# Optimization experiments

Hardware: AMD Instinct MI355X
Metric: run time of the kernel (lower is better)

The kernel has to match this reference:

```python
import jax, jax.numpy as jnp
import numpy as np

N, DIM, H, E = 50000, 64, 8, 800000
NEG_SLOPE = 0.2


def setup_inputs() -> dict:
    key = jax.random.key(0)
    ks = jax.random.split(key, 6)
    x = jax.random.normal(ks[0], (N, DIM), dtype=jnp.float32)
    edge_index = jax.random.randint(ks[1], (2, E), 0, N, dtype=jnp.int32)
    # glorot-ish scaled params
    W = jax.random.normal(ks[2], (DIM, H * DIM), dtype=jnp.float32) * (1.0 / np.sqrt(DIM))
    att_src = jax.random.normal(ks[3], (H, DIM), dtype=jnp.float32) * (1.0 / np.sqrt(DIM))
    att_dst = jax.random.normal(ks[4], (H, DIM), dtype=jnp.float32) * (1.0 / np.sqrt(DIM))
    bias = jnp.zeros((DIM,), dtype=jnp.float32)
    return {"x": x, "edge_index": edge_index, "W": W, "att_src": att_src, "att_dst": att_dst, "bias": bias}


def reference(x, edge_index, W, att_src, att_dst, bias):
    n = x.shape[0]
    # PyG GATConv default: add self-loops
    loops = jnp.arange(n, dtype=edge_index.dtype)
    src = jnp.concatenate([edge_index[0], loops])  # [E+N]
    dst = jnp.concatenate([edge_index[1], loops])  # [E+N]
    # project: [N, H, C]
    h = (x @ W).reshape(n, H, DIM)
    # per-node attention contributions: [N, H]
    a_src = jnp.einsum("nhc,hc->nh", h, att_src)
    a_dst = jnp.einsum("nhc,hc->nh", h, att_dst)
    # per-edge logits with LeakyReLU: [E+N, H]
    logits = jax.nn.leaky_relu(a_src[src] + a_dst[dst], negative_slope=NEG_SLOPE)
    # segment softmax over incoming edges of each destination node
    seg_max = jax.ops.segment_max(logits, dst, num_segments=n)  # [N, H]
    seg_max = jnp.where(jnp.isfinite(seg_max), seg_max, 0.0)
    e = jnp.exp(logits - seg_max[dst])
    denom = jax.ops.segment_sum(e, dst, num_segments=n)  # [N, H]
    alpha = e / denom[dst]  # every node has a self-loop -> denom > 0
    # weighted messages and scatter-add: [E+N, H, C] -> [N, H, C]
    msg = h[src] * alpha[:, :, None]
    out = jax.ops.segment_sum(msg, dst, num_segments=n)
    # concat=False -> mean over heads, then bias
    return out.mean(axis=1) + bias
```

## Files before the change

kernel.cpp:

```cpp
#include <hip/hip_runtime.h>
#include <hip/hip_bf16.h>

#define NHEAD 8
#define KDIM 64
#define NCOL 512
#define NEG_SLOPE 0.2f
#define BUCKET 62
#define ROWS 64
#define EPT 16

typedef short bf16x8 __attribute__((ext_vector_type(8)));
typedef float f32x4 __attribute__((ext_vector_type(4)));

__device__ inline float leaky(float x) { return fmaxf(x, NEG_SLOPE * x); }
__device__ inline float bf2f(unsigned short u) { return __uint_as_float(((unsigned)u) << 16); }
__device__ inline unsigned short f2bf(float f) {
    unsigned b = __float_as_uint(f);
    b += 0x7FFFu + ((b >> 16) & 1u);
    return (unsigned short)(b >> 16);
}

__global__ void k_wprep(const float* __restrict__ W, const float* __restrict__ att_src,
                        const float* __restrict__ att_dst,
                        float* __restrict__ WsT, float* __restrict__ WdT,
                        unsigned short* __restrict__ Bhi, unsigned short* __restrict__ Blo,
                        unsigned short* __restrict__ bucket, int n) {
    int tid = blockIdx.x * 256 + threadIdx.x;
    for (int i = tid; i < n; i += 32768) *(int*)(bucket + (size_t)i * ROWS) = 0;
    if (tid < NHEAD * KDIM) {
        int h = tid >> 6, k = tid & 63;
        float ps = 0.f, pd = 0.f;
        const float4* wp = (const float4*)(W + (size_t)k * NCOL + h * KDIM);
        const float4* sp = (const float4*)(att_src + h * KDIM);
        const float4* dp = (const float4*)(att_dst + h * KDIM);
        #pragma unroll
        for (int q = 0; q < KDIM / 4; ++q) {
            float4 wv = wp[q], sv = sp[q], dv = dp[q];
            ps += wv.x * sv.x + wv.y * sv.y + wv.z * sv.z + wv.w * sv.w;
            pd += wv.x * dv.x + wv.y * dv.y + wv.z * dv.z + wv.w * dv.w;
        }
        WsT[h * KDIM + k] = ps;
        WdT[h * KDIM + k] = pd;
    }
    if (tid < 4 * 16 * 64 * 8) {
        int j  = tid & 7;
        int l  = (tid >> 3) & 63;
        int kk = (tid >> 9) & 15;
        int ct = tid >> 13;
        int c  = ct * 16 + (l & 15);
        int hk = kk * 32 + ((l >> 4) << 3) + j;
        int h = hk >> 6, kx = hk & 63;
        float w = W[(size_t)kx * NCOL + h * KDIM + c];
        unsigned short hi = f2bf(w);
        Bhi[tid] = hi;
        Blo[tid] = f2bf(w - bf2f(hi));
    }
}

__global__ void k_xafill(const float* __restrict__ x,
                         const int* __restrict__ src, const int* __restrict__ dst,
                         const float* __restrict__ WsT, const float* __restrict__ WdT,
                         float* __restrict__ asrc, float* __restrict__ adst,
                         unsigned short* __restrict__ xb,
                         unsigned short* __restrict__ bucket,
                         int n, int E, int nbx) {
    const int b = blockIdx.x;
    const int t = threadIdx.x;
    if (b < nbx) {
        int i = b * 256 + t;
        if (i >= n * NHEAD) return;
        int node = i >> 3, h = i & 7;
        const float4* xp = (const float4*)(x + (size_t)node * KDIM);
        const float4* sp = (const float4*)(WsT + h * KDIM);
        const float4* dp = (const float4*)(WdT + h * KDIM);
        float ps = 0.f, pd = 0.f;
        float4 kept0 = {0, 0, 0, 0}, kept1 = {0, 0, 0, 0};
        #pragma unroll
        for (int q = 0; q < KDIM / 4; ++q) {
            float4 xv = xp[q], sv = sp[q], dv = dp[q];
            if (q == 2 * h)     kept0 = xv;
            if (q == 2 * h + 1) kept1 = xv;
            ps += xv.x * sv.x + xv.y * sv.y + xv.z * sv.z + xv.w * sv.w;
            pd += xv.x * dv.x + xv.y * dv.y + xv.z * dv.z + xv.w * dv.w;
        }
        asrc[i] = ps;
        adst[i] = pd;
        ushort4 o0, o1;
        o0.x = f2bf(kept0.x); o0.y = f2bf(kept0.y); o0.z = f2bf(kept0.z); o0.w = f2bf(kept0.w);
        o1.x = f2bf(kept1.x); o1.y = f2bf(kept1.y); o1.z = f2bf(kept1.z); o1.w = f2bf(kept1.w);
        ushort4* op = (ushort4*)(xb + (size_t)node * KDIM + h * 8);
        op[0] = o0; op[1] = o1;
    } else {
        long long base = ((long long)(b - nbx) * 256 + t) * EPT;
        if (base + EPT <= E) {
            int dd[EPT], ss[EPT], pp[EPT];
            #pragma unroll
            for (int q = 0; q < EPT; q += 4) {
                int4 dv = *(const int4*)(dst + base + q);
                int4 sv = *(const int4*)(src + base + q);
                dd[q] = dv.x; dd[q + 1] = dv.y; dd[q + 2] = dv.z; dd[q + 3] = dv.w;
                ss[q] = sv.x; ss[q + 1] = sv.y; ss[q + 2] = sv.z; ss[q + 3] = sv.w;
            }
            #pragma unroll
            for (int q = 0; q < EPT; ++q)
                pp[q] = atomicAdd((int*)(bucket + (size_t)dd[q] * ROWS), 1);
            #pragma unroll
            for (int q = 0; q < EPT; ++q)
                if (pp[q] < BUCKET)
                    bucket[(size_t)dd[q] * ROWS + 2 + pp[q]] = (unsigned short)ss[q];
        } else {
            for (long long i = base; i < E; ++i) {
                int d = dst[i];
                int p = atomicAdd((int*)(bucket + (size_t)d * ROWS), 1);
                if (p < BUCKET) bucket[(size_t)d * ROWS + 2 + p] = (unsigned short)src[i];
            }
        }
    }
}

__global__ __launch_bounds__(256, 8) void k_aggproj(const unsigned short* __restrict__ bucket,
                                                    const float* __restrict__ asrc,
                                                    const float* __restrict__ adst,
                                                    const unsigned short* __restrict__ xb,
                                                    const unsigned short* __restrict__ Bhi,
                                                    const unsigned short* __restrict__ Blo,
                                                    const float* __restrict__ bias,
                                                    float* __restrict__ out, int n) {
    __shared__ __align__(16) unsigned short Yh_l[16][520];

    const int t = threadIdx.x;
    const int w = t >> 6;
    const int lane = t & 63;
    const int base = blockIdx.x * 16;
    const int hg = lane >> 3;
    const int hLo = lane & 7;
    const int dly = (lane & 7) << 3;

#define PROCU(EV, RW)                                                          \
    {                                                                          \
        den += (EV);                                                           \
        uint4 u_ = (RW);                                                       \
        y[0] += (EV) * __uint_as_float(u_.x << 16);                            \
        y[1] += (EV) * __uint_as_float(u_.x & 0xFFFF0000u);                    \
        y[2] += (EV) * __uint_as_float(u_.y << 16);                            \
        y[3] += (EV) * __uint_as_float(u_.y & 0xFFFF0000u);                    \
        y[4] += (EV) * __uint_as_float(u_.z << 16);                            \
        y[5] += (EV) * __uint_as_float(u_.z & 0xFFFF0000u);                    \
        y[6] += (EV) * __uint_as_float(u_.w << 16);                            \
        y[7] += (EV) * __uint_as_float(u_.w & 0xFFFF0000u);                    \
    }

    for (int q = 0; q < 4; ++q) {
        const int row = w * 4 + q;
        int d = base + row;
        if (d >= n) d = n - 1;

        const float adLo = adst[(size_t)d * NHEAD + hLo];
        float den = 0.f;
        float y[8];
        #pragma unroll
        for (int i = 0; i < 8; ++i) y[i] = 0.f;

        const unsigned short* brow = bucket + (size_t)d * ROWS;
        int cnt = *(const int*)brow;
        cnt = cnt < BUCKET ? cnt : BUCKET;
        int sv = (lane < cnt) ? (int)brow[2 + lane] : 0;

        {
            float asLo = asrc[(size_t)d * NHEAD + hLo];
            float evs = __expf(leaky(asLo + adLo));
            float e = __shfl(evs, hg);
            uint4 r = *(const uint4*)(xb + ((size_t)d << 6) + dly);
            PROCU(e, r)
        }

        int j = 0;
        for (; j + 4 <= cnt; j += 4) {
            int sb = __shfl(sv, j + ((lane >> 3) & 3));
            float ab = asrc[(size_t)sb * NHEAD + hLo];
            float ev = __expf(leaky(ab + adLo));
            int s0 = __shfl(sv, j);
            int s1 = __shfl(sv, j + 1);
            int s2 = __shfl(sv, j + 2);
            int s3 = __shfl(sv, j + 3);
            uint4 r0 = *(const uint4*)(xb + ((size_t)s0 << 6) + dly);
            uint4 r1 = *(const uint4*)(xb + ((size_t)s1 << 6) + dly);
            uint4 r2 = *(const uint4*)(xb + ((size_t)s2 << 6) + dly);
            uint4 r3 = *(const uint4*)(xb + ((size_t)s3 << 6) + dly);
            float e0 = __shfl(ev, 0 * 8 + hg);
            PROCU(e0, r0)
            float e1 = __shfl(ev, 1 * 8 + hg);
            PROCU(e1, r1)
            float e2 = __shfl(ev, 2 * 8 + hg);
            PROCU(e2, r2)
            float e3 = __shfl(ev, 3 * 8 + hg);
            PROCU(e3, r3)
        }
        for (; j < cnt; ++j) {
            int s = __shfl(sv, j);
            float a = asrc[(size_t)s * NHEAD + hLo];
            float evt = __expf(leaky(a + adLo));
            float e = __shfl(evt, hg);
            uint4 r = *(const uint4*)(xb + ((size_t)s << 6) + dly);
            PROCU(e, r)
        }

        float inv = 1.0f / den;
        ushort4 h0, h1;
        h0.x = f2bf(y[0] * inv); h0.y = f2bf(y[1] * inv);
        h0.z = f2bf(y[2] * inv); h0.w = f2bf(y[3] * inv);
        h1.x = f2bf(y[4] * inv); h1.y = f2bf(y[5] * inv);
        h1.z = f2bf(y[6] * inv); h1.w = f2bf(y[7] * inv);
        unsigned short* yh = &Yh_l[row][hg * KDIM + dly];
        ((ushort4*)yh)[0] = h0; ((ushort4*)yh)[1] = h1;
    }
#undef PROCU

    __syncthreads();

    const bf16x8* BH = (const bf16x8*)Bhi;
    const bf16x8* BL = (const bf16x8*)Blo;
    const int ar = lane & 15;
    const int ak = (lane >> 4) << 3;

    f32x4 acc = {0.f, 0.f, 0.f, 0.f};
    #pragma unroll
    for (int kk = 0; kk < 16; ++kk) {
        bf16x8 ah = *(const bf16x8*)&Yh_l[ar][kk * 32 + ak];
        bf16x8 bh = BH[(w * 16 + kk) * 64 + lane];
        bf16x8 bl = BL[(w * 16 + kk) * 64 + lane];
        acc = __builtin_amdgcn_mfma_f32_16x16x32_bf16(ah, bh, acc, 0, 0, 0);
        acc = __builtin_amdgcn_mfma_f32_16x16x32_bf16(ah, bl, acc, 0, 0, 0);
    }

    int col = w * 16 + (lane & 15);
    float b = bias[col];
    int rbase = base + ((lane >> 4) << 2);
    #pragma unroll
    for (int r = 0; r < 4; ++r) {
        int rowg = rbase + r;
        if (rowg < n) out[(size_t)rowg * KDIM + col] = acc[r] * 0.125f + b;
    }
}

extern "C" void kernel_launch(void* const* d_in, const int* in_sizes, int n_in,
                              void* d_out, int out_size, void* d_ws, size_t ws_size,
                              hipStream_t stream) {
    const float* x       = (const float*)d_in[0];
    const int*   ei      = (const int*)d_in[1];
    const float* W       = (const float*)d_in[2];
    const float* att_src = (const float*)d_in[3];
    const float* att_dst = (const float*)d_in[4];
    const float* bias    = (const float*)d_in[5];

    const int n = in_sizes[0] / KDIM;
    const int E = in_sizes[1] / 2;
    const int* src = ei;
    const int* dst = ei + E;

    char* w = (char*)d_ws;
    unsigned short* xb  = (unsigned short*)w;  w += (size_t)n * KDIM * 2;
    unsigned short* Bhi = (unsigned short*)w;  w += (size_t)32768 * 2;
    unsigned short* Blo = (unsigned short*)w;  w += (size_t)32768 * 2;
    float* WsT  = (float*)w;                   w += (size_t)NHEAD * KDIM * 4;
    float* WdT  = (float*)w;                   w += (size_t)NHEAD * KDIM * 4;
    float* asrc = (float*)w;                   w += (size_t)n * NHEAD * 4;
    float* adst = (float*)w;                   w += (size_t)n * NHEAD * 4;
    w = (char*)(((size_t)w + 127) & ~(size_t)127);
    unsigned short* bucket = (unsigned short*)w; w += (size_t)n * ROWS * 2;

    k_wprep<<<128, 256, 0, stream>>>(W, att_src, att_dst, WsT, WdT, Bhi, Blo, bucket, n);

    const int nbx = (n * NHEAD + 255) / 256;
    const int ethreads = (E + EPT - 1) / EPT;
    const int nbe = (ethreads + 255) / 256;
    k_xafill<<<nbx + nbe, 256, 0, stream>>>(x, src, dst, WsT, WdT, asrc, adst, xb,
                                            bucket, n, E, nbx);

    k_aggproj<<<(n + 15) / 16, 256, 0, stream>>>(bucket, asrc, adst, xb, Bhi, Blo,
                                                 bias, (float*)d_out, n);
}
```

Baseline: 134.4 us.

## Fold weight-prep kernel into fill kernel and memset bucket counters

Removes the separate k_wprep launch. Each node-projection block now recomputes the folded W·att vectors into shared memory, and extra blocks at the end of k_xafill build the bf16 hi/lo B tiles. The bucket counters are cleared with a hipMemsetAsync over the whole bucket array instead of per-row int stores. The edge-bucketing blocks are placed first. This trades a kernel launch and a dependency for redundant per-block W·att work (512 dot products per block across ~1563 blocks) and a larger memset of 6.4 MB.

```diff
diff --git a/kernel.cpp b/kernel.cpp
--- a/kernel.cpp
+++ b/kernel.cpp
@@ -20,78 +20,19 @@
     return (unsigned short)(b >> 16);
 }
 
-__global__ void k_wprep(const float* __restrict__ W, const float* __restrict__ att_src,
-                        const float* __restrict__ att_dst,
-                        float* __restrict__ WsT, float* __restrict__ WdT,
-                        unsigned short* __restrict__ Bhi, unsigned short* __restrict__ Blo,
-                        unsigned short* __restrict__ bucket, int n) {
-    int tid = blockIdx.x * 256 + threadIdx.x;
-    for (int i = tid; i < n; i += 32768) *(int*)(bucket + (size_t)i * ROWS) = 0;
-    if (tid < NHEAD * KDIM) {
-        int h = tid >> 6, k = tid & 63;
-        float ps = 0.f, pd = 0.f;
-        const float4* wp = (const float4*)(W + (size_t)k * NCOL + h * KDIM);
-        const float4* sp = (const float4*)(att_src + h * KDIM);
-        const float4* dp = (const float4*)(att_dst + h * KDIM);
-        #pragma unroll
-        for (int q = 0; q < KDIM / 4; ++q) {
-            float4 wv = wp[q], sv = sp[q], dv = dp[q];
-            ps += wv.x * sv.x + wv.y * sv.y + wv.z * sv.z + wv.w * sv.w;
-            pd += wv.x * dv.x + wv.y * dv.y + wv.z * dv.z + wv.w * dv.w;
-        }
-        WsT[h * KDIM + k] = ps;
-        WdT[h * KDIM + k] = pd;
-    }
-    if (tid < 4 * 16 * 64 * 8) {
-        int j  = tid & 7;
-        int l  = (tid >> 3) & 63;
-        int kk = (tid >> 9) & 15;
-        int ct = tid >> 13;
-        int c  = ct * 16 + (l & 15);
-        int hk = kk * 32 + ((l >> 4) << 3) + j;
-        int h = hk >> 6, kx = hk & 63;
-        float w = W[(size_t)kx * NCOL + h * KDIM + c];
-        unsigned short hi = f2bf(w);
-        Bhi[tid] = hi;
-        Blo[tid] = f2bf(w - bf2f(hi));
-    }
-}
-
-__global__ void k_xafill(const float* __restrict__ x,
+__global__ void k_xafill(const float* __restrict__ x, const float* __restrict__ W,
+                         const float* __restrict__ att_src, const float* __restrict__ att_dst,
                          const int* __restrict__ src, const int* __restrict__ dst,
-                         const float* __restrict__ WsT, const float* __restrict__ WdT,
                          float* __restrict__ asrc, float* __restrict__ adst,
                          unsigned short* __restrict__ xb,
                          unsigned short* __restrict__ bucket,
-                         int n, int E, int nbx) {
+                         unsigned short* __restrict__ Bhi, unsigned short* __restrict__ Blo,
+                         int n, int E, int nbe, int nbx) {
     const int b = blockIdx.x;
     const int t = threadIdx.x;
-    if (b < nbx) {
-        int i = b * 256 + t;
-        if (i >= n * NHEAD) return;
-        int node = i >> 3, h = i & 7;
-        const float4* xp = (const float4*)(x + (size_t)node * KDIM);
-        const float4* sp = (const float4*)(WsT + h * KDIM);
-        const float4* dp = (const float4*)(WdT + h * KDIM);
-        float ps = 0.f, pd = 0.f;
-        float4 kept0 = {0, 0, 0, 0}, kept1 = {0, 0, 0, 0};
-        #pragma unroll
-        for (int q = 0; q < KDIM / 4; ++q) {
-            float4 xv = xp[q], sv = sp[q], dv = dp[q];
-            if (q == 2 * h)     kept0 = xv;
-            if (q == 2 * h + 1) kept1 = xv;
-            ps += xv.x * sv.x + xv.y * sv.y + xv.z * sv.z + xv.w * sv.w;
-            pd += xv.x * dv.x + xv.y * dv.y + xv.z * dv.z + xv.w * dv.w;
-        }
-        asrc[i] = ps;
-        adst[i] = pd;
-        ushort4 o0, o1;
-        o0.x = f2bf(kept0.x); o0.y = f2bf(kept0.y); o0.z = f2bf(kept0.z); o0.w = f2bf(kept0.w);
-        o1.x = f2bf(kept1.x); o1.y = f2bf(kept1.y); o1.z = f2bf(kept1.z); o1.w = f2bf(kept1.w);
-        ushort4* op = (ushort4*)(xb + (size_t)node * KDIM + h * 8);
-        op[0] = o0; op[1] = o1;
-    } else {
-        long long base = ((long long)(b - nbx) * 256 + t) * EPT;
+
+    if (b < nbe) {
+        long long base = ((long long)b * 256 + t) * EPT;
         if (base + EPT <= E) {
             int dd[EPT], ss[EPT], pp[EPT];
             #pragma unroll
@@ -114,6 +55,68 @@
                 int p = atomicAdd((int*)(bucket + (size_t)d * ROWS), 1);
                 if (p < BUCKET) bucket[(size_t)d * ROWS + 2 + p] = (unsigned short)src[i];
             }
+        }
+    } else if (b < nbe + nbx) {
+        __shared__ float WsT_l[NHEAD * KDIM];
+        __shared__ float WdT_l[NHEAD * KDIM];
+        #pragma unroll
+        for (int e = t; e < NHEAD * KDIM; e += 256) {
+            int h = e >> 6, k = e & 63;
+            float ps = 0.f, pd = 0.f;
+            const float4* wp = (const float4*)(W + (size_t)k * NCOL + h * KDIM);
+            const float4* sp = (const float4*)(att_src + h * KDIM);
+            const float4* dp = (const float4*)(att_dst + h * KDIM);
+            #pragma unroll
+            for (int q = 0; q < KDIM / 4; ++q) {
+                float4 wv = wp[q], sv = sp[q], dv = dp[q];
+                ps += wv.x * sv.x + wv.y * sv.y + wv.z * sv.z + wv.w * sv.w;
+                pd += wv.x * dv.x + wv.y * dv.y + wv.z * dv.z + wv.w * dv.w;
+            }
+            WsT_l[e] = ps;
+            WdT_l[e] = pd;
+        }
+        __syncthreads();
+
+        int i = (b - nbe) * 256 + t;
+        if (i < n * NHEAD) {
+            int node = i >> 3, h = i & 7;
+            const float4* xp = (const float4*)(x + (size_t)node * KDIM);
+            const float4* sp = (const float4*)(WsT_l + h * KDIM);
+            const float4* dp = (const float4*)(WdT_l + h * KDIM);
+            float ps = 0.f, pd = 0.f;
+            float4 kept0 = {0, 0, 0, 0}, kept1 = {0, 0, 0, 0};
+            #pragma unroll
+            for (int q = 0; q < KDIM / 4; ++q) {
+                float4 xv = xp[q], sv = sp[q], dv = dp[q];
+                if (q == 2 * h)     kept0 = xv;
+                if (q == 2 * h + 1) kept1 = xv;
+                ps += xv.x * sv.x + xv.y * sv.y + xv.z * sv.z + xv.w * sv.w;
+                pd += xv.x * dv.x + xv.y * dv.y + xv.z * dv.z + xv.w * dv.w;
+            }
+            asrc[i] = ps;
+            adst[i] = pd;
+            ushort4 o0, o1;
+            o0.x = f2bf(kept0.x); o0.y = f2bf(kept0.y);
+            o0.z = f2bf(kept0.z); o0.w = f2bf(kept0.w);
+            o1.x = f2bf(kept1.x); o1.y = f2bf(kept1.y);
+            o1.z = f2bf(kept1.z); o1.w = f2bf(kept1.w);
+            ushort4* op = (ushort4*)(xb + (size_t)node * KDIM + h * 8);
+            op[0] = o0; op[1] = o1;
+        }
+    } else {
+        int tid = (b - nbe - nbx) * 256 + t;
+        if (tid < 4 * 16 * 64 * 8) {
+            int j  = tid & 7;
+            int l  = (tid >> 3) & 63;
+            int kk = (tid >> 9) & 15;
+            int ct = tid >> 13;
+            int c  = ct * 16 + (l & 15);
+            int hk = kk * 32 + ((l >> 4) << 3) + j;
+            int h = hk >> 6, kx = hk & 63;
+            float w = W[(size_t)kx * NCOL + h * KDIM + c];
+            unsigned short hi = f2bf(w);
+            Bhi[tid] = hi;
+            Blo[tid] = f2bf(w - bf2f(hi));
         }
     }
 }
@@ -262,20 +265,19 @@
     unsigned short* xb  = (unsigned short*)w;  w += (size_t)n * KDIM * 2;
     unsigned short* Bhi = (unsigned short*)w;  w += (size_t)32768 * 2;
     unsigned short* Blo = (unsigned short*)w;  w += (size_t)32768 * 2;
-    float* WsT  = (float*)w;                   w += (size_t)NHEAD * KDIM * 4;
-    float* WdT  = (float*)w;                   w += (size_t)NHEAD * KDIM * 4;
     float* asrc = (float*)w;                   w += (size_t)n * NHEAD * 4;
     float* adst = (float*)w;                   w += (size_t)n * NHEAD * 4;
     w = (char*)(((size_t)w + 127) & ~(size_t)127);
     unsigned short* bucket = (unsigned short*)w; w += (size_t)n * ROWS * 2;
 
-    k_wprep<<<128, 256, 0, stream>>>(W, att_src, att_dst, WsT, WdT, Bhi, Blo, bucket, n);
-
-    const int nbx = (n * NHEAD + 255) / 256;
+    hipMemsetAsync(bucket, 0, (size_t)n * ROWS * 2, stream);
+
     const int ethreads = (E + EPT - 1) / EPT;
     const int nbe = (ethreads + 255) / 256;
-    k_xafill<<<nbx + nbe, 256, 0, stream>>>(x, src, dst, WsT, WdT, asrc, adst, xb,
-                                            bucket, n, E, nbx);
+    const int nbx = (n * NHEAD + 255) / 256;
+    k_xafill<<<nbe + nbx + 128, 256, 0, stream>>>(x, W, att_src, att_dst, src, dst,
+                                                  asrc, adst, xb, bucket, Bhi, Blo,
+                                                  n, E, nbe, nbx);
 
     k_aggproj<<<(n + 15) / 16, 256, 0, stream>>>(bucket, asrc, adst, xb, Bhi, Blo,
                                                  bias, (float*)d_out, n);
```

Measured after the change: 147.5 us. 1.1x slower.
